# Performance work log

Hardware: AMD Instinct MI355X
Metric: run time of the kernel (lower is better)

The kernel has to match this reference:

```python
import jax, jax.numpy as jnp
import numpy as np

N_NODES = 40000
N_EDGES = 640000
HIDDEN = 128
N_LAYERS = 4
N_CLASSES = 40
SCALING = HIDDEN ** -0.5  # num_heads = 1 -> head_dim = HIDDEN


def setup_inputs() -> dict:
    key = jax.random.key(0)
    ks = jax.random.split(key, 8)
    w_scale = HIDDEN ** -0.5
    h = jax.random.normal(ks[0], (N_NODES, HIDDEN), dtype=jnp.float32)
    src = jax.random.randint(ks[1], (N_EDGES,), 0, N_NODES, dtype=jnp.int32)
    dst = jnp.sort(jax.random.randint(ks[2], (N_EDGES,), 0, N_NODES, dtype=jnp.int32))
    Wq = jax.random.normal(ks[3], (N_LAYERS, HIDDEN, HIDDEN), dtype=jnp.float32) * w_scale
    Wk = jax.random.normal(ks[4], (N_LAYERS, HIDDEN, HIDDEN), dtype=jnp.float32) * w_scale
    Wv = jax.random.normal(ks[5], (N_LAYERS, HIDDEN, HIDDEN), dtype=jnp.float32) * w_scale
    bq = jnp.zeros((N_LAYERS, HIDDEN), dtype=jnp.float32)
    bk = jnp.zeros((N_LAYERS, HIDDEN), dtype=jnp.float32)
    bv = jnp.zeros((N_LAYERS, HIDDEN), dtype=jnp.float32)
    Wout = jax.random.normal(ks[6], (HIDDEN, N_CLASSES), dtype=jnp.float32) * w_scale
    bout = jnp.zeros((N_CLASSES,), dtype=jnp.float32)
    return {"h": h, "src": src, "dst": dst, "Wq": Wq, "bq": bq, "Wk": Wk,
            "bk": bk, "Wv": Wv, "bv": bv, "Wout": Wout, "bout": bout}


def _edge_softmax_spmm(q, k, v, src, dst):
    """Sparse MHA over graph edges (num_heads=1).
    score_e = <q[dst_e], k[src_e]>, softmax over incoming edges per dst,
    out[i] = sum_{e: dst_e = i} attn_e * v[src_e].
    """
    # SDDMM: [E]
    score = jnp.einsum('ed,ed->e', q[dst], k[src])
    # edge softmax over destination segments (stable)
    m = jax.ops.segment_max(score, dst, num_segments=N_NODES)  # [N]
    e = jnp.exp(score - m[dst])                                # [E]
    s = jax.ops.segment_sum(e, dst, num_segments=N_NODES)      # [N]
    attn = e / jnp.maximum(s[dst], 1e-20)                      # [E]
    # SpMM: [N, d]
    return jax.ops.segment_sum(attn[:, None] * v[src], dst, num_segments=N_NODES)


def reference(h, src, dst, Wq, bq, Wk, bk, Wv, bv, Wout, bout):
    for l in range(N_LAYERS):
        q = (h @ Wq[l] + bq[l]) * SCALING
        k = h @ Wk[l] + bk[l]
        v = h @ Wv[l] + bv[l]
        h = _edge_softmax_spmm(q, k, v, src, dst)
    logits = h @ Wout + bout
    return jax.nn.log_softmax(logits, axis=-1)
```

## Files before the change

kernel.cpp:

```cpp
#include <hip/hip_runtime.h>
#include <math.h>

#define N_NODES 40000
#define N_EDGES 640000
#define HIDDEN 128
#define N_LAYERS 4
#define N_CLASSES 40
#define SCALING 0.08838834764831845f

typedef __attribute__((ext_vector_type(8))) short short8;
typedef __attribute__((ext_vector_type(4))) float floatx4;

static __device__ __forceinline__ float b2f(unsigned short u) {
  return __uint_as_float(((unsigned)u) << 16);
}
static __device__ __forceinline__ unsigned short f2b(float f) {
  unsigned u = __float_as_uint(f);
  u += 0x7fff + ((u >> 16) & 1);
  return (unsigned short)(u >> 16);
}

__global__ __launch_bounds__(256) void setup_all(
    const float* __restrict__ h_in, const int* __restrict__ dst,
    unsigned short* __restrict__ g0, int* __restrict__ row_start)
{
  int idx = blockIdx.x * 256 + threadIdx.x;
  if (idx < 640000) {
    const float4* p = (const float4*)h_in + (size_t)idx * 2;
    float4 a = p[0], b = p[1];
    union { unsigned short us[8]; uint4 v; } o;
    o.us[0] = f2b(a.x); o.us[1] = f2b(a.y); o.us[2] = f2b(a.z); o.us[3] = f2b(a.w);
    o.us[4] = f2b(b.x); o.us[5] = f2b(b.y); o.us[6] = f2b(b.z); o.us[7] = f2b(b.w);
    ((uint4*)g0)[idx] = o.v;
    return;
  }
  int c = idx - 640000;
  if (c <= N_NODES) {
    int lo = 0, hi = N_EDGES;
    while (lo < hi) {
      int mid = (lo + hi) >> 1;
      if (dst[mid] < c) lo = mid + 1; else hi = mid;
    }
    row_start[c] = lo;
  }
}

struct MMJob {
  const float* A; const float* B;
  float* Cf; unsigned short* Cb;
  float scale;
  int abt; int ncolsB; int storeT; int padrows;
};
struct MMStage { MMJob jobs[4]; int njobs; int bias; };

__global__ __launch_bounds__(256) void mm_stage(
    MMStage st,
    const float* __restrict__ Wq, const float* __restrict__ Wk,
    const float* __restrict__ Wv, const float* __restrict__ Wout,
    const float* __restrict__ bq, const float* __restrict__ bv,
    const float* __restrict__ bout,
    const float* __restrict__ C2, const float* __restrict__ C3,
    float* __restrict__ zb, float* __restrict__ bout2)
{
  int blk = blockIdx.x;
  if (blk < st.njobs * 64) {
    MMJob J = st.jobs[blk >> 6];
    int bi = blk & 63;
    int ty = threadIdx.x >> 7;
    int c  = threadIdx.x & 127;
    int r  = bi * 2 + ty;
    float acc = 0.f;
    if (J.abt) {
      const float* ar = J.A + (size_t)r * 128;
      const float* br = J.B + (size_t)c * 128;
      #pragma unroll 4
      for (int j = 0; j < 128; ++j) acc += ar[j] * br[j];
    } else if (c < J.ncolsB) {
      const float* ar = J.A + (size_t)r * 128;
      #pragma unroll 4
      for (int j = 0; j < 128; ++j) acc += ar[j] * J.B[(size_t)j * J.ncolsB + c];
    }
    acc *= J.scale;
    if (J.storeT) {
      if (c < J.ncolsB) {
        if (J.Cb) J.Cb[(size_t)c * 128 + r] = f2b(acc);
        else      J.Cf[(size_t)c * 128 + r] = acc;
      } else if (c < J.padrows && J.Cb) {
        J.Cb[(size_t)c * 128 + r] = 0;
      }
    } else if (c < J.ncolsB) {
      if (J.Cb) J.Cb[(size_t)r * J.ncolsB + c] = f2b(acc);
      else      J.Cf[(size_t)r * J.ncolsB + c] = acc;
    }
    return;
  }
  if (!st.bias) return;

  int t = threadIdx.x;
  __shared__ float cb[128], v1[128], v2[128], cbn[128];
  if (t < 128) {
    const float* wk0 = Wk + (size_t)t * 128;
    float s = 0.f;
    for (int o = 0; o < 128; ++o) s += bq[o] * wk0[o];
    zb[t] = s * SCALING;
    cb[t] = bv[t];
  }
  __syncthreads();
  for (int l = 1; l < 4; ++l) {
    const float* Cvl = (l == 1) ? Wv : (l == 2 ? C2 : C3);
    if (t < 128) {
      float s = bq[(size_t)l * 128 + t];
      for (int o = 0; o < 128; ++o) s += cb[o] * Wq[(size_t)l * 16384 + (size_t)o * 128 + t];
      v1[t] = s;
    }
    __syncthreads();
    if (t < 128) {
      float s = 0.f;
      const float* wkr = Wk + (size_t)l * 16384 + (size_t)t * 128;
      for (int o = 0; o < 128; ++o) s += v1[o] * wkr[o];
      v2[t] = s;
    }
    __syncthreads();
    if (t < 128) {
      float s = 0.f;
      const float* cvr = Cvl + (size_t)t * 128;
      for (int d = 0; d < 128; ++d) s += v2[d] * cvr[d];
      zb[(size_t)l * 128 + t] = s * SCALING;
      float s2 = bv[(size_t)l * 128 + t];
      for (int d = 0; d < 128; ++d) s2 += cb[d] * Wv[(size_t)l * 16384 + (size_t)d * 128 + t];
      cbn[t] = s2;
    }
    __syncthreads();
    if (t < 128) cb[t] = cbn[t];
    __syncthreads();
  }
  if (t < N_CLASSES) {
    float s = bout[t];
    for (int d = 0; d < 128; ++d) s += cb[d] * Wout[(size_t)d * N_CLASSES + t];
    bout2[t] = s;
  }
}

__global__ __launch_bounds__(256) void gemm_z(
    const unsigned short* __restrict__ A,
    const unsigned short* __restrict__ Wt,
    const float* __restrict__ bias,
    unsigned short* __restrict__ C)
{
  constexpr int ROWB = 256;
  __shared__ __align__(16) unsigned char cs[32 * ROWB];

  const int tid = threadIdx.x;
  const int wid = tid >> 6, lane = tid & 63;
  const int r = lane & 15, kg = lane >> 4;
  const int colhalf = wid & 1, rowsub = wid >> 1;
  const int colbase = colhalf * 64;
  const int ro = rowsub * 16 + r;
  const int row = blockIdx.x * 32 + ro;

  short8 hf[4];
  #pragma unroll
  for (int kc = 0; kc < 4; ++kc)
    hf[kc] = *(const short8*)(A + (size_t)row * 128 + kc * 32 + kg * 8);

  floatx4 acc[4];
  #pragma unroll
  for (int df = 0; df < 4; ++df) acc[df] = (floatx4){0.f, 0.f, 0.f, 0.f};

  const unsigned short* wp = Wt + (size_t)(colbase + r) * 128 + kg * 8;
  #pragma unroll
  for (int df = 0; df < 4; ++df) {
    #pragma unroll
    for (int kc = 0; kc < 4; ++kc) {
      short8 wf = *(const short8*)(wp + df * 2048 + kc * 32);
      acc[df] = __builtin_amdgcn_mfma_f32_16x16x32_bf16(wf, hf[kc], acc[df], 0, 0, 0);
    }
  }

  #pragma unroll
  for (int df = 0; df < 4; ++df) {
    float4 b4 = *(const float4*)&bias[colbase + df * 16 + kg * 4];
    union { unsigned short us[4]; uint2 u2; } o;
    o.us[0] = f2b(acc[df][0] + b4.x);
    o.us[1] = f2b(acc[df][1] + b4.y);
    o.us[2] = f2b(acc[df][2] + b4.z);
    o.us[3] = f2b(acc[df][3] + b4.w);
    int colb = (colbase + df * 16 + kg * 4) * 2;
    *(uint2*)(cs + ro * ROWB + (colb ^ ((ro & 7) << 4))) = o.u2;
  }
  __syncthreads();

  unsigned char* dstb = (unsigned char*)(C + (size_t)blockIdx.x * 32 * 128);
  #pragma unroll
  for (int i = 0; i < 2; ++i) {
    int byte = (i * 256 + tid) * 16;
    int ro2 = byte / ROWB;
    int colb2 = byte & (ROWB - 1);
    *(uint4*)(dstb + byte) =
        *(const uint4*)(cs + ro2 * ROWB + (colb2 ^ ((ro2 & 7) << 4)));
  }
}

__global__ __launch_bounds__(128) void edge_fused(
    const unsigned short* __restrict__ z, const unsigned short* __restrict__ g,
    const int* __restrict__ src, const int* __restrict__ row_start,
    unsigned short* __restrict__ gout)
{
  const int lane = threadIdx.x & 63;
  const int node = blockIdx.x * 2 + (threadIdx.x >> 6);
  const int sg = lane >> 4, sl = lane & 15;

  short8 qf = *(const short8*)(z + ((size_t)node << 7) + sl * 8);
  float qd[8];
  #pragma unroll
  for (int j = 0; j < 8; ++j) qd[j] = b2f((unsigned short)qf[j]);

  const int r0 = row_start[node], r1 = row_start[node + 1];

  float acc[8] = {0.f, 0.f, 0.f, 0.f, 0.f, 0.f, 0.f, 0.f};
  float ws = 0.f;

#define LOADG(VLD, HF, C)                                               \
  {                                                                     \
    int e_ = (C) + sg;                                                  \
    VLD = e_ < r1;                                                      \
    int s_ = VLD ? src[e_] : 0;                                         \
    HF = *(const short8*)(g + ((size_t)s_ << 7) + sl * 8);              \
  }

#define COMPG(VLD, HF)                                                  \
  {                                                                     \
    float hd_[8];                                                       \
    _Pragma("unroll")                                                   \
    for (int j = 0; j < 8; ++j) hd_[j] = b2f((unsigned short)HF[j]);    \
    float d0_ = 0.f, d1_ = 0.f;                                         \
    _Pragma("unroll")                                                   \
    for (int j = 0; j < 4; ++j) d0_ += qd[j] * hd_[j];                  \
    _Pragma("unroll")                                                   \
    for (int j = 4; j < 8; ++j) d1_ += qd[j] * hd_[j];                  \
    float d_ = d0_ + d1_;                                               \
    d_ += __shfl_xor(d_, 1, 64);                                        \
    d_ += __shfl_xor(d_, 2, 64);                                        \
    d_ += __shfl_xor(d_, 4, 64);                                        \
    d_ += __shfl_xor(d_, 8, 64);                                        \
    float w_ = VLD ? __expf(d_) : 0.f;                                  \
    ws += w_;                                                           \
    _Pragma("unroll")                                                   \
    for (int j = 0; j < 8; ++j) acc[j] += w_ * hd_[j];                  \
  }

  bool vA, vB;
  short8 hA, hB;
  LOADG(vA, hA, r0);
  LOADG(vB, hB, r0 + 4);

  for (int c = r0; c < r1; c += 8) {
    bool vC, vD;
    short8 hC, hD;
    LOADG(vC, hC, c + 8);
    LOADG(vD, hD, c + 12);
    COMPG(vA, hA);
    COMPG(vB, hB);
    vA = vC; hA = hC;
    vB = vD; hB = hD;
  }

#undef LOADG
#undef COMPG

  #pragma unroll
  for (int off = 16; off <= 32; off <<= 1) {
    ws += __shfl_xor(ws, off, 64);
    #pragma unroll
    for (int j = 0; j < 8; ++j) acc[j] += __shfl_xor(acc[j], off, 64);
  }

  if (sg == 0) {
    float inv = (ws > 1e-20f) ? 1.0f / ws : 0.0f;
    union { unsigned short us[8]; uint4 u4; } o;
    #pragma unroll
    for (int j = 0; j < 8; ++j) o.us[j] = f2b(acc[j] * inv);
    *(uint4*)(gout + (size_t)node * 128 + sl * 8) = o.u4;
  }
}

__global__ __launch_bounds__(256) void out_head_mfma(
    const unsigned short* __restrict__ h, const unsigned short* __restrict__ wout_t,
    const float* __restrict__ bout, float* __restrict__ out)
{
  __shared__ __align__(16) float os[64 * N_CLASSES];

  const int wid = threadIdx.x >> 6, lane = threadIdx.x & 63;
  const int r = lane & 15, kg = lane >> 4;
  const int row_base = blockIdx.x * 64 + wid * 16;
  const int ar = row_base + r;

  floatx4 acc[3];
  #pragma unroll
  for (int n = 0; n < 3; ++n) acc[n] = (floatx4){0.f, 0.f, 0.f, 0.f};

  const unsigned short* ap = h + (size_t)ar * 128 + kg * 8;
  const unsigned short* bp = wout_t + (size_t)r * 128 + kg * 8;

  #pragma unroll
  for (int kc = 0; kc < 128; kc += 32) {
    short8 a0 = *(const short8*)(ap + kc);
    #pragma unroll
    for (int n = 0; n < 3; ++n) {
      short8 b = *(const short8*)(bp + n * 2048 + kc);
      acc[n] = __builtin_amdgcn_mfma_f32_16x16x32_bf16(a0, b, acc[n], 0, 0, 0);
    }
  }

  float bn0 = bout[r];
  float bn1 = bout[16 + r];
  float bn2 = (r < 8) ? bout[32 + r] : 0.f;

  #pragma unroll
  for (int g = 0; g < 4; ++g) {
    int rl = wid * 16 + kg * 4 + g;
    float l0 = acc[0][g] + bn0;
    float l1 = acc[1][g] + bn1;
    float l2 = acc[2][g] + bn2;
    float m = fmaxf(l0, l1);
    if (r < 8) m = fmaxf(m, l2);
    #pragma unroll
    for (int off = 8; off >= 1; off >>= 1) m = fmaxf(m, __shfl_xor(m, off, 64));
    float s = __expf(l0 - m) + __expf(l1 - m) + ((r < 8) ? __expf(l2 - m) : 0.f);
    #pragma unroll
    for (int off = 8; off >= 1; off >>= 1) s += __shfl_xor(s, off, 64);
    float lse = m + logf(s);
    os[rl * N_CLASSES + r]      = l0 - lse;
    os[rl * N_CLASSES + 16 + r] = l1 - lse;
    if (r < 8) os[rl * N_CLASSES + 32 + r] = l2 - lse;
  }
  __syncthreads();

  float* dstb = out + (size_t)blockIdx.x * 64 * N_CLASSES;
  #pragma unroll
  for (int i = 0; i < 3; ++i) {
    int idx = i * 256 + threadIdx.x;
    if (idx < 640)
      *(uint4*)(dstb + idx * 4) = *(const uint4*)(os + idx * 4);
  }
}

extern "C" void kernel_launch(void* const* d_in, const int* in_sizes, int n_in,
                              void* d_out, int out_size, void* d_ws, size_t ws_size,
                              hipStream_t stream) {
  const float* h_in = (const float*)d_in[0];
  const int*   src  = (const int*)d_in[1];
  const int*   dst  = (const int*)d_in[2];
  const float* Wq   = (const float*)d_in[3];
  const float* bq   = (const float*)d_in[4];
  const float* Wk   = (const float*)d_in[5];
  const float* bk   = (const float*)d_in[6];
  const float* Wv   = (const float*)d_in[7];
  const float* bv   = (const float*)d_in[8];
  const float* Wout = (const float*)d_in[9];
  const float* bout = (const float*)d_in[10];
  float* out = (float*)d_out;
  (void)bk;

  char* ws = (char*)d_ws;
  size_t off = 0;
  auto alloc = [&](size_t bytes) -> void* {
    void* p = ws + off;
    off += (bytes + 255) & ~(size_t)255;
    return p;
  };
  int*            row_start = (int*)           alloc((size_t)(N_NODES + 1) * sizeof(int));
  unsigned short* g0        = (unsigned short*)alloc((size_t)N_NODES * 128 * 2);
  unsigned short* g1        = (unsigned short*)alloc((size_t)N_NODES * 128 * 2);
  unsigned short* zbuf      = (unsigned short*)alloc((size_t)N_NODES * 128 * 2);
  unsigned short* WZ        = (unsigned short*)alloc((size_t)4 * 16384 * 2);
  unsigned short* WOt       = (unsigned short*)alloc((size_t)48 * 128 * 2);
  float*          C2        = (float*)alloc(16384 * sizeof(float));
  float*          C3        = (float*)alloc(16384 * sizeof(float));
  float*          C4        = (float*)alloc(16384 * sizeof(float));
  float*          Abuf      = (float*)alloc(3 * 16384 * sizeof(float));
  float*          Bbuf      = (float*)alloc(3 * 16384 * sizeof(float));
  float*          zb        = (float*)alloc(4 * 128 * sizeof(float));
  float*          bout2     = (float*)alloc(64 * sizeof(float));

  setup_all<<<(680001 + 255) / 256, 256, 0, stream>>>(h_in, dst, g0, row_start);

  auto J = [](const float* A, const float* B, float* Cf, unsigned short* Cb,
              float scale, int abt, int ncolsB, int storeT, int padrows) {
    MMJob j; j.A = A; j.B = B; j.Cf = Cf; j.Cb = Cb; j.scale = scale;
    j.abt = abt; j.ncolsB = ncolsB; j.storeT = storeT; j.padrows = padrows;
    return j;
  };
  const float* Wq_l[4] = {Wq, Wq + 16384, Wq + 32768, Wq + 49152};
  const float* Wk_l[4] = {Wk, Wk + 16384, Wk + 32768, Wk + 49152};
  const float* Wv_l[4] = {Wv, Wv + 16384, Wv + 32768, Wv + 49152};

  MMStage s0 = {};
  s0.jobs[0] = J(Wk_l[0], Wq_l[0], nullptr, WZ, SCALING, 1, 128, 0, 0);
  s0.jobs[1] = J(Wv_l[0], Wv_l[1], C2, nullptr, 1.f, 0, 128, 0, 0);
  s0.jobs[2] = J(Wv_l[0], Wk_l[1], Abuf, nullptr, 1.f, 0, 128, 0, 0);
  s0.jobs[3] = J(Wv_l[0], Wq_l[1], Bbuf, nullptr, 1.f, 0, 128, 0, 0);
  s0.njobs = 4; s0.bias = 0;

  MMStage s1 = {};
  s1.jobs[0] = J(Abuf, Bbuf, nullptr, WZ + 16384, SCALING, 1, 128, 0, 0);
  s1.jobs[1] = J(C2, Wv_l[2], C3, nullptr, 1.f, 0, 128, 0, 0);
  s1.jobs[2] = J(C2, Wk_l[2], Abuf + 16384, nullptr, 1.f, 0, 128, 0, 0);
  s1.jobs[3] = J(C2, Wq_l[2], Bbuf + 16384, nullptr, 1.f, 0, 128, 0, 0);
  s1.njobs = 4; s1.bias = 0;

  MMStage s2 = {};
  s2.jobs[0] = J(Abuf + 16384, Bbuf + 16384, nullptr, WZ + 32768, SCALING, 1, 128, 0, 0);
  s2.jobs[1] = J(C3, Wv_l[3], C4, nullptr, 1.f, 0, 128, 0, 0);
  s2.jobs[2] = J(C3, Wk_l[3], Abuf + 32768, nullptr, 1.f, 0, 128, 0, 0);
  s2.jobs[3] = J(C3, Wq_l[3], Bbuf + 32768, nullptr, 1.f, 0, 128, 0, 0);
  s2.njobs = 4; s2.bias = 0;

  MMStage s3 = {};
  s3.jobs[0] = J(Abuf + 32768, Bbuf + 32768, nullptr, WZ + 49152, SCALING, 1, 128, 0, 0);
  s3.jobs[1] = J(C4, Wout, nullptr, WOt, 1.f, 0, N_CLASSES, 1, 48);
  s3.njobs = 2; s3.bias = 1;

  mm_stage<<<4 * 64, 256, 0, stream>>>(s0, Wq, Wk, Wv, Wout, bq, bv, bout, C2, C3, zb, bout2);
  mm_stage<<<4 * 64, 256, 0, stream>>>(s1, Wq, Wk, Wv, Wout, bq, bv, bout, C2, C3, zb, bout2);
  mm_stage<<<4 * 64, 256, 0, stream>>>(s2, Wq, Wk, Wv, Wout, bq, bv, bout, C2, C3, zb, bout2);
  mm_stage<<<2 * 64 + 1, 256, 0, stream>>>(s3, Wq, Wk, Wv, Wout, bq, bv, bout, C2, C3, zb, bout2);

  unsigned short* gcur = g0;
  unsigned short* gnext = g1;
  for (int l = 0; l < N_LAYERS; ++l) {
    gemm_z<<<1250, 256, 0, stream>>>(gcur, WZ + (size_t)l * 16384, zb + (size_t)l * 128, zbuf);
    edge_fused<<<N_NODES / 2, 128, 0, stream>>>(zbuf, gcur, src, row_start, gnext);
    unsigned short* tmp = gcur; gcur = gnext; gnext = tmp;
  }
  out_head_mfma<<<625, 256, 0, stream>>>(gcur, WOt, bout2, out);
}
```

Before: 251.5 us.

## Fuse per-layer GEMM into edge aggregation kernel and fold output head into last layer

Merges the gemm_z and edge_fused kernels so each 256-thread block computes the projected query rows for 32 nodes into shared memory and then aggregates neighbours for those nodes. This avoids writing and rereading the z buffer in global memory and saves launches. The final layer keeps its outputs in shared memory and applies the output head with log-softmax in the same kernel. In exchange, each wave now processes 8 nodes serially instead of 1 node per wave across 20000 blocks, which reduces parallelism for latency hiding on the gather and adds load imbalance from varying node degrees.

```diff
diff --git a/kernel.cpp b/kernel.cpp
--- a/kernel.cpp
+++ b/kernel.cpp
@@ -141,89 +141,70 @@
   }
 }
 
-__global__ __launch_bounds__(256) void gemm_z(
-    const unsigned short* __restrict__ A,
+template<bool LAST>
+__global__ __launch_bounds__(256) void layer_fused(
+    const unsigned short* __restrict__ g,
     const unsigned short* __restrict__ Wt,
     const float* __restrict__ bias,
-    unsigned short* __restrict__ C)
+    const int* __restrict__ src, const int* __restrict__ row_start,
+    unsigned short* __restrict__ gout,
+    const unsigned short* __restrict__ WOt,
+    const float* __restrict__ bout2,
+    float* __restrict__ out)
 {
-  constexpr int ROWB = 256;
-  __shared__ __align__(16) unsigned char cs[32 * ROWB];
+  __shared__ __align__(16) unsigned char zs[8192];
+  __shared__ __align__(16) unsigned char gs2[LAST ? 8192 : 16];
+  __shared__ __align__(16) float os[LAST ? 32 * N_CLASSES : 4];
 
   const int tid = threadIdx.x;
   const int wid = tid >> 6, lane = tid & 63;
   const int r = lane & 15, kg = lane >> 4;
-  const int colhalf = wid & 1, rowsub = wid >> 1;
-  const int colbase = colhalf * 64;
-  const int ro = rowsub * 16 + r;
-  const int row = blockIdx.x * 32 + ro;
-
-  short8 hf[4];
-  #pragma unroll
-  for (int kc = 0; kc < 4; ++kc)
-    hf[kc] = *(const short8*)(A + (size_t)row * 128 + kc * 32 + kg * 8);
-
-  floatx4 acc[4];
-  #pragma unroll
-  for (int df = 0; df < 4; ++df) acc[df] = (floatx4){0.f, 0.f, 0.f, 0.f};
-
-  const unsigned short* wp = Wt + (size_t)(colbase + r) * 128 + kg * 8;
-  #pragma unroll
-  for (int df = 0; df < 4; ++df) {
-    #pragma unroll
-    for (int kc = 0; kc < 4; ++kc) {
-      short8 wf = *(const short8*)(wp + df * 2048 + kc * 32);
-      acc[df] = __builtin_amdgcn_mfma_f32_16x16x32_bf16(wf, hf[kc], acc[df], 0, 0, 0);
-    }
-  }
-
-  #pragma unroll
-  for (int df = 0; df < 4; ++df) {
-    float4 b4 = *(const float4*)&bias[colbase + df * 16 + kg * 4];
-    union { unsigned short us[4]; uint2 u2; } o;
-    o.us[0] = f2b(acc[df][0] + b4.x);
-    o.us[1] = f2b(acc[df][1] + b4.y);
-    o.us[2] = f2b(acc[df][2] + b4.z);
-    o.us[3] = f2b(acc[df][3] + b4.w);
-    int colb = (colbase + df * 16 + kg * 4) * 2;
-    *(uint2*)(cs + ro * ROWB + (colb ^ ((ro & 7) << 4))) = o.u2;
+
+  {
+    const int colhalf = wid & 1, rowsub = wid >> 1;
+    const int colbase = colhalf * 64;
+    const int ro = rowsub * 16 + r;
+    const int row = blockIdx.x * 32 + ro;
+
+    short8 hf[4];
+    #pragma unroll
+    for (int kc = 0; kc < 4; ++kc)
+      hf[kc] = *(const short8*)(g + (size_t)row * 128 + kc * 32 + kg * 8);
+
+    floatx4 acc[4];
+    #pragma unroll
+    for (int df = 0; df < 4; ++df) acc[df] = (floatx4){0.f, 0.f, 0.f, 0.f};
+
+    const unsigned short* wp = Wt + (size_t)(colbase + r) * 128 + kg * 8;
+    #pragma unroll
+    for (int df = 0; df < 4; ++df) {
+      #pragma unroll
+      for (int kc = 0; kc < 4; ++kc) {
+        short8 wf = *(const short8*)(wp + df * 2048 + kc * 32);
+        acc[df] = __builtin_amdgcn_mfma_f32_16x16x32_bf16(wf, hf[kc], acc[df], 0, 0, 0);
+      }
+    }
+
+    #pragma unroll
+    for (int df = 0; df < 4; ++df) {
+      float4 b4 = *(const float4*)&bias[colbase + df * 16 + kg * 4];
+      union { unsigned short us[4]; uint2 u2; } o;
+      o.us[0] = f2b(acc[df][0] + b4.x);
+      o.us[1] = f2b(acc[df][1] + b4.y);
+      o.us[2] = f2b(acc[df][2] + b4.z);
+      o.us[3] = f2b(acc[df][3] + b4.w);
+      int colb = (colbase + df * 16 + kg * 4) * 2;
+      *(uint2*)(zs + ro * 256 + (colb ^ ((ro & 7) << 4))) = o.u2;
+    }
   }
   __syncthreads();
 
-  unsigned char* dstb = (unsigned char*)(C + (size_t)blockIdx.x * 32 * 128);
-  #pragma unroll
-  for (int i = 0; i < 2; ++i) {
-    int byte = (i * 256 + tid) * 16;
-    int ro2 = byte / ROWB;
-    int colb2 = byte & (ROWB - 1);
-    *(uint4*)(dstb + byte) =
-        *(const uint4*)(cs + ro2 * ROWB + (colb2 ^ ((ro2 & 7) << 4)));
-  }
-}
-
-__global__ __launch_bounds__(128) void edge_fused(
-    const unsigned short* __restrict__ z, const unsigned short* __restrict__ g,
-    const int* __restrict__ src, const int* __restrict__ row_start,
-    unsigned short* __restrict__ gout)
-{
-  const int lane = threadIdx.x & 63;
-  const int node = blockIdx.x * 2 + (threadIdx.x >> 6);
   const int sg = lane >> 4, sl = lane & 15;
 
-  short8 qf = *(const short8*)(z + ((size_t)node << 7) + sl * 8);
-  float qd[8];
-  #pragma unroll
-  for (int j = 0; j < 8; ++j) qd[j] = b2f((unsigned short)qf[j]);
-
-  const int r0 = row_start[node], r1 = row_start[node + 1];
-
-  float acc[8] = {0.f, 0.f, 0.f, 0.f, 0.f, 0.f, 0.f, 0.f};
-  float ws = 0.f;
-
-#define LOADG(VLD, HF, C)                                               \
+#define LOADG(VLD, HF, C, R1)                                           \
   {                                                                     \
     int e_ = (C) + sg;                                                  \
-    VLD = e_ < r1;                                                      \
+    VLD = e_ < R1;                                                      \
     int s_ = VLD ? src[e_] : 0;                                         \
     HF = *(const short8*)(g + ((size_t)s_ << 7) + sl * 8);              \
   }
@@ -249,98 +230,109 @@
     for (int j = 0; j < 8; ++j) acc[j] += w_ * hd_[j];                  \
   }
 
-  bool vA, vB;
-  short8 hA, hB;
-  LOADG(vA, hA, r0);
-  LOADG(vB, hB, r0 + 4);
-
-  for (int c = r0; c < r1; c += 8) {
-    bool vC, vD;
-    short8 hC, hD;
-    LOADG(vC, hC, c + 8);
-    LOADG(vD, hD, c + 12);
-    COMPG(vA, hA);
-    COMPG(vB, hB);
-    vA = vC; hA = hC;
-    vB = vD; hB = hD;
+  for (int ni = 0; ni < 8; ++ni) {
+    const int nl = wid * 8 + ni;
+    const int node = blockIdx.x * 32 + nl;
+
+    short8 qf = *(const short8*)(zs + nl * 256 + ((sl * 16) ^ ((nl & 7) << 4)));
+    float qd[8];
+    #pragma unroll
+    for (int j = 0; j < 8; ++j) qd[j] = b2f((unsigned short)qf[j]);
+
+    const int r0 = row_start[node], r1 = row_start[node + 1];
+
+    float acc[8] = {0.f, 0.f, 0.f, 0.f, 0.f, 0.f, 0.f, 0.f};
+    float ws = 0.f;
+
+    bool vA, vB;
+    short8 hA, hB;
+    LOADG(vA, hA, r0, r1);
+    LOADG(vB, hB, r0 + 4, r1);
+
+    for (int c = r0; c < r1; c += 8) {
+      bool vC, vD;
+      short8 hC, hD;
+      LOADG(vC, hC, c + 8, r1);
+      LOADG(vD, hD, c + 12, r1);
+      COMPG(vA, hA);
+      COMPG(vB, hB);
+      vA = vC; hA = hC;
+      vB = vD; hB = hD;
+    }
+
+    #pragma unroll
+    for (int off = 16; off <= 32; off <<= 1) {
+      ws += __shfl_xor(ws, off, 64);
+      #pragma unroll
+      for (int j = 0; j < 8; ++j) acc[j] += __shfl_xor(acc[j], off, 64);
+    }
+
+    if (sg == 0) {
+      float inv = (ws > 1e-20f) ? 1.0f / ws : 0.0f;
+      union { unsigned short us[8]; uint4 u4; } o;
+      #pragma unroll
+      for (int j = 0; j < 8; ++j) o.us[j] = f2b(acc[j] * inv);
+      if (LAST)
+        *(uint4*)(gs2 + nl * 256 + ((sl * 16) ^ ((nl & 7) << 4))) = o.u4;
+      else
+        *(uint4*)(gout + (size_t)node * 128 + sl * 8) = o.u4;
+    }
   }
 
 #undef LOADG
 #undef COMPG
 
+  if (!LAST) return;
+
+  __syncthreads();
+  if (wid < 2) {
+    const int rowl = wid * 16 + r;
+    floatx4 acc[3];
+    #pragma unroll
+    for (int n = 0; n < 3; ++n) acc[n] = (floatx4){0.f, 0.f, 0.f, 0.f};
+
+    const unsigned short* bp = WOt + (size_t)r * 128 + kg * 8;
+    #pragma unroll
+    for (int kc = 0; kc < 4; ++kc) {
+      short8 a0 = *(const short8*)(gs2 + rowl * 256 +
+                                   ((kc * 64 + kg * 16) ^ ((rowl & 7) << 4)));
+      #pragma unroll
+      for (int n = 0; n < 3; ++n) {
+        short8 b = *(const short8*)(bp + n * 2048 + kc * 32);
+        acc[n] = __builtin_amdgcn_mfma_f32_16x16x32_bf16(a0, b, acc[n], 0, 0, 0);
+      }
+    }
+
+    float bn0 = bout2[r];
+    float bn1 = bout2[16 + r];
+    float bn2 = (r < 8) ? bout2[32 + r] : 0.f;
+
+    #pragma unroll
+    for (int gi = 0; gi < 4; ++gi) {
+      int rl = wid * 16 + kg * 4 + gi;
+      float l0 = acc[0][gi] + bn0;
+      float l1 = acc[1][gi] + bn1;
+      float l2 = acc[2][gi] + bn2;
+      float m = fmaxf(l0, l1);
+      if (r < 8) m = fmaxf(m, l2);
+      #pragma unroll
+      for (int off = 8; off >= 1; off >>= 1) m = fmaxf(m, __shfl_xor(m, off, 64));
+      float s = __expf(l0 - m) + __expf(l1 - m) + ((r < 8) ? __expf(l2 - m) : 0.f);
+      #pragma unroll
+      for (int off = 8; off >= 1; off >>= 1) s += __shfl_xor(s, off, 64);
+      float lse = m + logf(s);
+      os[rl * N_CLASSES + r]      = l0 - lse;
+      os[rl * N_CLASSES + 16 + r] = l1 - lse;
+      if (r < 8) os[rl * N_CLASSES + 32 + r] = l2 - lse;
+    }
+  }
+  __syncthreads();
+
+  float* dstb = out + (size_t)blockIdx.x * 32 * N_CLASSES;
   #pragma unroll
-  for (int off = 16; off <= 32; off <<= 1) {
-    ws += __shfl_xor(ws, off, 64);
-    #pragma unroll
-    for (int j = 0; j < 8; ++j) acc[j] += __shfl_xor(acc[j], off, 64);
-  }
-
-  if (sg == 0) {
-    float inv = (ws > 1e-20f) ? 1.0f / ws : 0.0f;
-    union { unsigned short us[8]; uint4 u4; } o;
-    #pragma unroll
-    for (int j = 0; j < 8; ++j) o.us[j] = f2b(acc[j] * inv);
-    *(uint4*)(gout + (size_t)node * 128 + sl * 8) = o.u4;
-  }
-}
-
-__global__ __launch_bounds__(256) void out_head_mfma(
-    const unsigned short* __restrict__ h, const unsigned short* __restrict__ wout_t,
-    const float* __restrict__ bout, float* __restrict__ out)
-{
-  __shared__ __align__(16) float os[64 * N_CLASSES];
-
-  const int wid = threadIdx.x >> 6, lane = threadIdx.x & 63;
-  const int r = lane & 15, kg = lane >> 4;
-  const int row_base = blockIdx.x * 64 + wid * 16;
-  const int ar = row_base + r;
-
-  floatx4 acc[3];
-  #pragma unroll
-  for (int n = 0; n < 3; ++n) acc[n] = (floatx4){0.f, 0.f, 0.f, 0.f};
-
-  const unsigned short* ap = h + (size_t)ar * 128 + kg * 8;
-  const unsigned short* bp = wout_t + (size_t)r * 128 + kg * 8;
-
-  #pragma unroll
-  for (int kc = 0; kc < 128; kc += 32) {
-    short8 a0 = *(const short8*)(ap + kc);
-    #pragma unroll
-    for (int n = 0; n < 3; ++n) {
-      short8 b = *(const short8*)(bp + n * 2048 + kc);
-      acc[n] = __builtin_amdgcn_mfma_f32_16x16x32_bf16(a0, b, acc[n], 0, 0, 0);
-    }
-  }
-
-  float bn0 = bout[r];
-  float bn1 = bout[16 + r];
-  float bn2 = (r < 8) ? bout[32 + r] : 0.f;
-
-  #pragma unroll
-  for (int g = 0; g < 4; ++g) {
-    int rl = wid * 16 + kg * 4 + g;
-    float l0 = acc[0][g] + bn0;
-    float l1 = acc[1][g] + bn1;
-    float l2 = acc[2][g] + bn2;
-    float m = fmaxf(l0, l1);
-    if (r < 8) m = fmaxf(m, l2);
-    #pragma unroll
-    for (int off = 8; off >= 1; off >>= 1) m = fmaxf(m, __shfl_xor(m, off, 64));
-    float s = __expf(l0 - m) + __expf(l1 - m) + ((r < 8) ? __expf(l2 - m) : 0.f);
-    #pragma unroll
-    for (int off = 8; off >= 1; off >>= 1) s += __shfl_xor(s, off, 64);
-    float lse = m + logf(s);
-    os[rl * N_CLASSES + r]      = l0 - lse;
-    os[rl * N_CLASSES + 16 + r] = l1 - lse;
-    if (r < 8) os[rl * N_CLASSES + 32 + r] = l2 - lse;
-  }
-  __syncthreads();
-
-  float* dstb = out + (size_t)blockIdx.x * 64 * N_CLASSES;
-  #pragma unroll
-  for (int i = 0; i < 3; ++i) {
-    int idx = i * 256 + threadIdx.x;
-    if (idx < 640)
+  for (int i = 0; i < 2; ++i) {
+    int idx = i * 256 + tid;
+    if (idx < 320)
       *(uint4*)(dstb + idx * 4) = *(const uint4*)(os + idx * 4);
   }
 }
@@ -372,7 +364,6 @@
   int*            row_start = (int*)           alloc((size_t)(N_NODES + 1) * sizeof(int));
   unsigned short* g0        = (unsigned short*)alloc((size_t)N_NODES * 128 * 2);
   unsigned short* g1        = (unsigned short*)alloc((size_t)N_NODES * 128 * 2);
-  unsigned short* zbuf      = (unsigned short*)alloc((size_t)N_NODES * 128 * 2);
   unsigned short* WZ        = (unsigned short*)alloc((size_t)4 * 16384 * 2);
   unsigned short* WOt       = (unsigned short*)alloc((size_t)48 * 128 * 2);
   float*          C2        = (float*)alloc(16384 * sizeof(float));
@@ -426,12 +417,12 @@
   mm_stage<<<4 * 64, 256, 0, stream>>>(s2, Wq, Wk, Wv, Wout, bq, bv, bout, C2, C3, zb, bout2);
   mm_stage<<<2 * 64 + 1, 256, 0, stream>>>(s3, Wq, Wk, Wv, Wout, bq, bv, bout, C2, C3, zb, bout2);
 
-  unsigned short* gcur = g0;
-  unsigned short* gnext = g1;
-  for (int l = 0; l < N_LAYERS; ++l) {
-    gemm_z<<<1250, 256, 0, stream>>>(gcur, WZ + (size_t)l * 16384, zb + (size_t)l * 128, zbuf);
-    edge_fused<<<N_NODES / 2, 128, 0, stream>>>(zbuf, gcur, src, row_start, gnext);
-    unsigned short* tmp = gcur; gcur = gnext; gnext = tmp;
-  }
-  out_head_mfma<<<625, 256, 0, stream>>>(gcur, WOt, bout2, out);
-}
+  layer_fused<false><<<1250, 256, 0, stream>>>(
+      g0, WZ, zb, src, row_start, g1, nullptr, nullptr, nullptr);
+  layer_fused<false><<<1250, 256, 0, stream>>>(
+      g1, WZ + 16384, zb + 128, src, row_start, g0, nullptr, nullptr, nullptr);
+  layer_fused<false><<<1250, 256, 0, stream>>>(
+      g0, WZ + 32768, zb + 256, src, row_start, g1, nullptr, nullptr, nullptr);
+  layer_fused<true><<<1250, 256, 0, stream>>>(
+      g1, WZ + 49152, zb + 384, src, row_start, nullptr, WOt, bout2, out);
+}
```

New measurement: 254.9 us. About the same (+1.4%).

## Fuse weight folding stages, layer-0 gemm, and output head into fewer launches

Applied to the files above, without the earlier changes.

Restructures the weight-product chain into a shallower dependency tree: Wv2·Wv3 and the layer-3 partial products are computed in parallel in the first stage, and the stages are merged with the setup kernel and the layer-0 z GEMM. This cuts kernel launches from 14 to 10. The final SpMM is fused with the output projection and log-softmax, so the last hidden state is never written to memory and the separate head kernel disappears. In exchange, the head is computed with scalar FMAs and shuffles instead of MFMA, and the fused kernels carry heterogeneous block roles.

```diff
diff --git a/kernel.cpp b/kernel.cpp
--- a/kernel.cpp
+++ b/kernel.cpp
@@ -20,124 +20,203 @@
   return (unsigned short)(u >> 16);
 }
 
-__global__ __launch_bounds__(256) void setup_all(
-    const float* __restrict__ h_in, const int* __restrict__ dst,
-    unsigned short* __restrict__ g0, int* __restrict__ row_start)
-{
-  int idx = blockIdx.x * 256 + threadIdx.x;
-  if (idx < 640000) {
-    const float4* p = (const float4*)h_in + (size_t)idx * 2;
-    float4 a = p[0], b = p[1];
-    union { unsigned short us[8]; uint4 v; } o;
-    o.us[0] = f2b(a.x); o.us[1] = f2b(a.y); o.us[2] = f2b(a.z); o.us[3] = f2b(a.w);
-    o.us[4] = f2b(b.x); o.us[5] = f2b(b.y); o.us[6] = f2b(b.z); o.us[7] = f2b(b.w);
-    ((uint4*)g0)[idx] = o.v;
-    return;
-  }
-  int c = idx - 640000;
-  if (c <= N_NODES) {
-    int lo = 0, hi = N_EDGES;
-    while (lo < hi) {
-      int mid = (lo + hi) >> 1;
-      if (dst[mid] < c) lo = mid + 1; else hi = mid;
-    }
-    row_start[c] = lo;
-  }
-}
-
 struct MMJob {
   const float* A; const float* B;
   float* Cf; unsigned short* Cb;
   float scale;
   int abt; int ncolsB; int storeT; int padrows;
 };
-struct MMStage { MMJob jobs[4]; int njobs; int bias; };
-
-__global__ __launch_bounds__(256) void mm_stage(
-    MMStage st,
+struct MM7 { MMJob j[7]; };
+struct MM3 { MMJob j[3]; };
+
+static __device__ __forceinline__ void run_job(const MMJob J, int bi) {
+  int ty = threadIdx.x >> 7;
+  int c  = threadIdx.x & 127;
+  int r  = bi * 2 + ty;
+  float acc = 0.f;
+  if (J.abt) {
+    const float* ar = J.A + (size_t)r * 128;
+    const float* br = J.B + (size_t)c * 128;
+    #pragma unroll 4
+    for (int j = 0; j < 128; ++j) acc += ar[j] * br[j];
+  } else if (c < J.ncolsB) {
+    const float* ar = J.A + (size_t)r * 128;
+    #pragma unroll 4
+    for (int j = 0; j < 128; ++j) acc += ar[j] * J.B[(size_t)j * J.ncolsB + c];
+  }
+  acc *= J.scale;
+  if (J.storeT) {
+    if (c < J.ncolsB) {
+      if (J.Cb) J.Cb[(size_t)c * 128 + r] = f2b(acc);
+      else      J.Cf[(size_t)c * 128 + r] = acc;
+    } else if (c < J.padrows && J.Cb) {
+      J.Cb[(size_t)c * 128 + r] = 0;
+    }
+  } else if (c < J.ncolsB) {
+    if (J.Cb) J.Cb[(size_t)r * J.ncolsB + c] = f2b(acc);
+    else      J.Cf[(size_t)r * J.ncolsB + c] = acc;
+  }
+}
+
+__global__ __launch_bounds__(256) void setup_fold1(
+    const float* __restrict__ h_in, const int* __restrict__ dst,
+    const float* __restrict__ bq, const float* __restrict__ Wk,
+    unsigned short* __restrict__ g0, int* __restrict__ row_start,
+    float* __restrict__ zb, MM7 st)
+{
+  int blk = blockIdx.x;
+  if (blk < 2657) {
+    int idx = blk * 256 + threadIdx.x;
+    if (idx < 640000) {
+      const float4* p = (const float4*)h_in + (size_t)idx * 2;
+      float4 a = p[0], b = p[1];
+      union { unsigned short us[8]; uint4 v; } o;
+      o.us[0] = f2b(a.x); o.us[1] = f2b(a.y); o.us[2] = f2b(a.z); o.us[3] = f2b(a.w);
+      o.us[4] = f2b(b.x); o.us[5] = f2b(b.y); o.us[6] = f2b(b.z); o.us[7] = f2b(b.w);
+      ((uint4*)g0)[idx] = o.v;
+      return;
+    }
+    int c = idx - 640000;
+    if (c <= N_NODES) {
+      int lo = 0, hi = N_EDGES;
+      while (lo < hi) {
+        int mid = (lo + hi) >> 1;
+        if (dst[mid] < c) lo = mid + 1; else hi = mid;
+      }
+      row_start[c] = lo;
+    }
+    return;
+  }
+  if (blk < 3105) {
+    int b2 = blk - 2657;
+    run_job(st.j[b2 >> 6], b2 & 63);
+    return;
+  }
+  int t = threadIdx.x;
+  if (t < 128) {
+    const float* wkr = Wk + (size_t)t * 128;
+    float s = 0.f;
+    #pragma unroll 4
+    for (int o = 0; o < 128; ++o) s += bq[o] * wkr[o];
+    zb[t] = s * SCALING;
+  }
+}
+
+__global__ __launch_bounds__(256) void fold2(MM7 st) {
+  run_job(st.j[blockIdx.x >> 6], blockIdx.x & 63);
+}
+
+__global__ __launch_bounds__(256) void fold3_z0(
+    MM3 st,
     const float* __restrict__ Wq, const float* __restrict__ Wk,
     const float* __restrict__ Wv, const float* __restrict__ Wout,
     const float* __restrict__ bq, const float* __restrict__ bv,
     const float* __restrict__ bout,
-    const float* __restrict__ C2, const float* __restrict__ C3,
-    float* __restrict__ zb, float* __restrict__ bout2)
+    const float* __restrict__ D01, const float* __restrict__ C3f,
+    float* __restrict__ zb, float* __restrict__ bout2,
+    const unsigned short* __restrict__ g, const unsigned short* __restrict__ WZ0,
+    unsigned short* __restrict__ zout)
 {
   int blk = blockIdx.x;
-  if (blk < st.njobs * 64) {
-    MMJob J = st.jobs[blk >> 6];
-    int bi = blk & 63;
-    int ty = threadIdx.x >> 7;
-    int c  = threadIdx.x & 127;
-    int r  = bi * 2 + ty;
-    float acc = 0.f;
-    if (J.abt) {
-      const float* ar = J.A + (size_t)r * 128;
-      const float* br = J.B + (size_t)c * 128;
-      #pragma unroll 4
-      for (int j = 0; j < 128; ++j) acc += ar[j] * br[j];
-    } else if (c < J.ncolsB) {
-      const float* ar = J.A + (size_t)r * 128;
-      #pragma unroll 4
-      for (int j = 0; j < 128; ++j) acc += ar[j] * J.B[(size_t)j * J.ncolsB + c];
-    }
-    acc *= J.scale;
-    if (J.storeT) {
-      if (c < J.ncolsB) {
-        if (J.Cb) J.Cb[(size_t)c * 128 + r] = f2b(acc);
-        else      J.Cf[(size_t)c * 128 + r] = acc;
-      } else if (c < J.padrows && J.Cb) {
-        J.Cb[(size_t)c * 128 + r] = 0;
+  if (blk < 192) {
+    run_job(st.j[blk >> 6], blk & 63);
+    return;
+  }
+  if (blk == 192) {
+    int t = threadIdx.x;
+    __shared__ float cb[128], v1[128], v2[128], cbn[128];
+    if (t < 128) cb[t] = bv[t];
+    __syncthreads();
+    for (int l = 1; l < 4; ++l) {
+      const float* Cvl = (l == 1) ? Wv : (l == 2 ? D01 : C3f);
+      if (t < 128) {
+        float s = bq[(size_t)l * 128 + t];
+        for (int o = 0; o < 128; ++o) s += cb[o] * Wq[(size_t)l * 16384 + (size_t)o * 128 + t];
+        v1[t] = s;
       }
-    } else if (c < J.ncolsB) {
-      if (J.Cb) J.Cb[(size_t)r * J.ncolsB + c] = f2b(acc);
-      else      J.Cf[(size_t)r * J.ncolsB + c] = acc;
+      __syncthreads();
+      if (t < 128) {
+        float s = 0.f;
+        const float* wkr = Wk + (size_t)l * 16384 + (size_t)t * 128;
+        for (int o = 0; o < 128; ++o) s += v1[o] * wkr[o];
+        v2[t] = s;
+      }
+      __syncthreads();
+      if (t < 128) {
+        float s = 0.f;
+        const float* cvr = Cvl + (size_t)t * 128;
+        for (int d = 0; d < 128; ++d) s += v2[d] * cvr[d];
+        zb[(size_t)l * 128 + t] = s * SCALING;
+        float s2 = bv[(size_t)l * 128 + t];
+        for (int d = 0; d < 128; ++d) s2 += cb[d] * Wv[(size_t)l * 16384 + (size_t)d * 128 + t];
+        cbn[t] = s2;
+      }
+      __syncthreads();
+      if (t < 128) cb[t] = cbn[t];
+      __syncthreads();
+    }
+    if (t < N_CLASSES) {
+      float s = bout[t];
+      for (int d = 0; d < 128; ++d) s += cb[d] * Wout[(size_t)d * N_CLASSES + t];
+      bout2[t] = s;
     }
     return;
   }
-  if (!st.bias) return;
-
-  int t = threadIdx.x;
-  __shared__ float cb[128], v1[128], v2[128], cbn[128];
-  if (t < 128) {
-    const float* wk0 = Wk + (size_t)t * 128;
-    float s = 0.f;
-    for (int o = 0; o < 128; ++o) s += bq[o] * wk0[o];
-    zb[t] = s * SCALING;
-    cb[t] = bv[t];
-  }
-  __syncthreads();
-  for (int l = 1; l < 4; ++l) {
-    const float* Cvl = (l == 1) ? Wv : (l == 2 ? C2 : C3);
-    if (t < 128) {
-      float s = bq[(size_t)l * 128 + t];
-      for (int o = 0; o < 128; ++o) s += cb[o] * Wq[(size_t)l * 16384 + (size_t)o * 128 + t];
-      v1[t] = s;
+
+  {
+    const int tile = blk - 193;
+    constexpr int ROWB = 256;
+    __shared__ __align__(16) unsigned char cs[32 * ROWB];
+
+    const int tid = threadIdx.x;
+    const int wid = tid >> 6, lane = tid & 63;
+    const int r = lane & 15, kg = lane >> 4;
+    const int colhalf = wid & 1, rowsub = wid >> 1;
+    const int colbase = colhalf * 64;
+    const int ro = rowsub * 16 + r;
+    const int row = tile * 32 + ro;
+
+    short8 hf[4];
+    #pragma unroll
+    for (int kc = 0; kc < 4; ++kc)
+      hf[kc] = *(const short8*)(g + (size_t)row * 128 + kc * 32 + kg * 8);
+
+    floatx4 acc[4];
+    #pragma unroll
+    for (int df = 0; df < 4; ++df) acc[df] = (floatx4){0.f, 0.f, 0.f, 0.f};
+
+    const unsigned short* wp = WZ0 + (size_t)(colbase + r) * 128 + kg * 8;
+    #pragma unroll
+    for (int df = 0; df < 4; ++df) {
+      #pragma unroll
+      for (int kc = 0; kc < 4; ++kc) {
+        short8 wf = *(const short8*)(wp + df * 2048 + kc * 32);
+        acc[df] = __builtin_amdgcn_mfma_f32_16x16x32_bf16(wf, hf[kc], acc[df], 0, 0, 0);
+      }
+    }
+
+    #pragma unroll
+    for (int df = 0; df < 4; ++df) {
+      float4 b4 = *(const float4*)&zb[colbase + df * 16 + kg * 4];
+      union { unsigned short us[4]; uint2 u2; } o;
+      o.us[0] = f2b(acc[df][0] + b4.x);
+      o.us[1] = f2b(acc[df][1] + b4.y);
+      o.us[2] = f2b(acc[df][2] + b4.z);
+      o.us[3] = f2b(acc[df][3] + b4.w);
+      int colb = (colbase + df * 16 + kg * 4) * 2;
+      *(uint2*)(cs + ro * ROWB + (colb ^ ((ro & 7) << 4))) = o.u2;
     }
     __syncthreads();
-    if (t < 128) {
-      float s = 0.f;
-      const float* wkr = Wk + (size_t)l * 16384 + (size_t)t * 128;
-      for (int o = 0; o < 128; ++o) s += v1[o] * wkr[o];
-      v2[t] = s;
-    }
-    __syncthreads();
-    if (t < 128) {
-      float s = 0.f;
-      const float* cvr = Cvl + (size_t)t * 128;
-      for (int d = 0; d < 128; ++d) s += v2[d] * cvr[d];
-      zb[(size_t)l * 128 + t] = s * SCALING;
-      float s2 = bv[(size_t)l * 128 + t];
-      for (int d = 0; d < 128; ++d) s2 += cb[d] * Wv[(size_t)l * 16384 + (size_t)d * 128 + t];
-      cbn[t] = s2;
-    }
-    __syncthreads();
-    if (t < 128) cb[t] = cbn[t];
-    __syncthreads();
-  }
-  if (t < N_CLASSES) {
-    float s = bout[t];
-    for (int d = 0; d < 128; ++d) s += cb[d] * Wout[(size_t)d * N_CLASSES + t];
-    bout2[t] = s;
+
+    unsigned char* dstb = (unsigned char*)(zout + (size_t)tile * 32 * 128);
+    #pragma unroll
+    for (int i = 0; i < 2; ++i) {
+      int byte = (i * 256 + tid) * 16;
+      int ro2 = byte / ROWB;
+      int colb2 = byte & (ROWB - 1);
+      *(uint4*)(dstb + byte) =
+          *(const uint4*)(cs + ro2 * ROWB + (colb2 ^ ((ro2 & 7) << 4)));
+    }
   }
 }
 
@@ -201,26 +280,7 @@
   }
 }
 
-__global__ __launch_bounds__(128) void edge_fused(
-    const unsigned short* __restrict__ z, const unsigned short* __restrict__ g,
-    const int* __restrict__ src, const int* __restrict__ row_start,
-    unsigned short* __restrict__ gout)
-{
-  const int lane = threadIdx.x & 63;
-  const int node = blockIdx.x * 2 + (threadIdx.x >> 6);
-  const int sg = lane >> 4, sl = lane & 15;
-
-  short8 qf = *(const short8*)(z + ((size_t)node << 7) + sl * 8);
-  float qd[8];
-  #pragma unroll
-  for (int j = 0; j < 8; ++j) qd[j] = b2f((unsigned short)qf[j]);
-
-  const int r0 = row_start[node], r1 = row_start[node + 1];
-
-  float acc[8] = {0.f, 0.f, 0.f, 0.f, 0.f, 0.f, 0.f, 0.f};
-  float ws = 0.f;
-
-#define LOADG(VLD, HF, C)                                               \
+#define EDGE_LOADG(VLD, HF, C)                                          \
   {                                                                     \
     int e_ = (C) + sg;                                                  \
     VLD = e_ < r1;                                                      \
@@ -228,7 +288,7 @@
     HF = *(const short8*)(g + ((size_t)s_ << 7) + sl * 8);              \
   }
 
-#define COMPG(VLD, HF)                                                  \
+#define EDGE_COMPG(VLD, HF)                                             \
   {                                                                     \
     float hd_[8];                                                       \
     _Pragma("unroll")                                                   \
@@ -249,31 +309,47 @@
     for (int j = 0; j < 8; ++j) acc[j] += w_ * hd_[j];                  \
   }
 
-  bool vA, vB;
-  short8 hA, hB;
-  LOADG(vA, hA, r0);
-  LOADG(vB, hB, r0 + 4);
-
-  for (int c = r0; c < r1; c += 8) {
-    bool vC, vD;
-    short8 hC, hD;
-    LOADG(vC, hC, c + 8);
-    LOADG(vD, hD, c + 12);
-    COMPG(vA, hA);
-    COMPG(vB, hB);
-    vA = vC; hA = hC;
-    vB = vD; hB = hD;
-  }
-
-#undef LOADG
-#undef COMPG
-
-  #pragma unroll
-  for (int off = 16; off <= 32; off <<= 1) {
-    ws += __shfl_xor(ws, off, 64);
-    #pragma unroll
-    for (int j = 0; j < 8; ++j) acc[j] += __shfl_xor(acc[j], off, 64);
-  }
+#define EDGE_BODY                                                       \
+  float acc[8] = {0.f, 0.f, 0.f, 0.f, 0.f, 0.f, 0.f, 0.f};              \
+  float ws = 0.f;                                                       \
+  bool vA, vB;                                                          \
+  short8 hA, hB;                                                        \
+  EDGE_LOADG(vA, hA, r0);                                               \
+  EDGE_LOADG(vB, hB, r0 + 4);                                           \
+  for (int c = r0; c < r1; c += 8) {                                    \
+    bool vC, vD;                                                        \
+    short8 hC, hD;                                                      \
+    EDGE_LOADG(vC, hC, c + 8);                                          \
+    EDGE_LOADG(vD, hD, c + 12);                                         \
+    EDGE_COMPG(vA, hA);                                                 \
+    EDGE_COMPG(vB, hB);                                                 \
+    vA = vC; hA = hC;                                                   \
+    vB = vD; hB = hD;                                                   \
+  }                                                                     \
+  _Pragma("unroll")                                                     \
+  for (int off = 16; off <= 32; off <<= 1) {                            \
+    ws += __shfl_xor(ws, off, 64);                                      \
+    _Pragma("unroll")                                                   \
+    for (int j = 0; j < 8; ++j) acc[j] += __shfl_xor(acc[j], off, 64);  \
+  }
+
+__global__ __launch_bounds__(128) void edge_fused(
+    const unsigned short* __restrict__ z, const unsigned short* __restrict__ g,
+    const int* __restrict__ src, const int* __restrict__ row_start,
+    unsigned short* __restrict__ gout)
+{
+  const int lane = threadIdx.x & 63;
+  const int node = blockIdx.x * 2 + (threadIdx.x >> 6);
+  const int sg = lane >> 4, sl = lane & 15;
+
+  short8 qf = *(const short8*)(z + ((size_t)node << 7) + sl * 8);
+  float qd[8];
+  #pragma unroll
+  for (int j = 0; j < 8; ++j) qd[j] = b2f((unsigned short)qf[j]);
+
+  const int r0 = row_start[node], r1 = row_start[node + 1];
+
+  EDGE_BODY
 
   if (sg == 0) {
     float inv = (ws > 1e-20f) ? 1.0f / ws : 0.0f;
@@ -284,66 +360,64 @@
   }
 }
 
-__global__ __launch_bounds__(256) void out_head_mfma(
-    const unsigned short* __restrict__ h, const unsigned short* __restrict__ wout_t,
-    const float* __restrict__ bout, float* __restrict__ out)
+__global__ __launch_bounds__(128) void edge_head(
+    const unsigned short* __restrict__ z, const unsigned short* __restrict__ g,
+    const int* __restrict__ src, const int* __restrict__ row_start,
+    const unsigned short* __restrict__ WOt, const float* __restrict__ bout2,
+    float* __restrict__ out)
 {
-  __shared__ __align__(16) float os[64 * N_CLASSES];
-
-  const int wid = threadIdx.x >> 6, lane = threadIdx.x & 63;
-  const int r = lane & 15, kg = lane >> 4;
-  const int row_base = blockIdx.x * 64 + wid * 16;
-  const int ar = row_base + r;
-
-  floatx4 acc[3];
-  #pragma unroll
-  for (int n = 0; n < 3; ++n) acc[n] = (floatx4){0.f, 0.f, 0.f, 0.f};
-
-  const unsigned short* ap = h + (size_t)ar * 128 + kg * 8;
-  const unsigned short* bp = wout_t + (size_t)r * 128 + kg * 8;
-
-  #pragma unroll
-  for (int kc = 0; kc < 128; kc += 32) {
-    short8 a0 = *(const short8*)(ap + kc);
-    #pragma unroll
-    for (int n = 0; n < 3; ++n) {
-      short8 b = *(const short8*)(bp + n * 2048 + kc);
-      acc[n] = __builtin_amdgcn_mfma_f32_16x16x32_bf16(a0, b, acc[n], 0, 0, 0);
-    }
-  }
-
-  float bn0 = bout[r];
-  float bn1 = bout[16 + r];
-  float bn2 = (r < 8) ? bout[32 + r] : 0.f;
-
-  #pragma unroll
-  for (int g = 0; g < 4; ++g) {
-    int rl = wid * 16 + kg * 4 + g;
-    float l0 = acc[0][g] + bn0;
-    float l1 = acc[1][g] + bn1;
-    float l2 = acc[2][g] + bn2;
-    float m = fmaxf(l0, l1);
-    if (r < 8) m = fmaxf(m, l2);
-    #pragma unroll
-    for (int off = 8; off >= 1; off >>= 1) m = fmaxf(m, __shfl_xor(m, off, 64));
-    float s = __expf(l0 - m) + __expf(l1 - m) + ((r < 8) ? __expf(l2 - m) : 0.f);
-    #pragma unroll
-    for (int off = 8; off >= 1; off >>= 1) s += __shfl_xor(s, off, 64);
-    float lse = m + logf(s);
-    os[rl * N_CLASSES + r]      = l0 - lse;
-    os[rl * N_CLASSES + 16 + r] = l1 - lse;
-    if (r < 8) os[rl * N_CLASSES + 32 + r] = l2 - lse;
-  }
-  __syncthreads();
-
-  float* dstb = out + (size_t)blockIdx.x * 64 * N_CLASSES;
-  #pragma unroll
-  for (int i = 0; i < 3; ++i) {
-    int idx = i * 256 + threadIdx.x;
-    if (idx < 640)
-      *(uint4*)(dstb + idx * 4) = *(const uint4*)(os + idx * 4);
-  }
-}
+  const int lane = threadIdx.x & 63;
+  const int node = blockIdx.x * 2 + (threadIdx.x >> 6);
+  const int sg = lane >> 4, sl = lane & 15;
+
+  short8 qf = *(const short8*)(z + ((size_t)node << 7) + sl * 8);
+  float qd[8];
+  #pragma unroll
+  for (int j = 0; j < 8; ++j) qd[j] = b2f((unsigned short)qf[j]);
+
+  const int r0 = row_start[node], r1 = row_start[node + 1];
+
+  EDGE_BODY
+
+  float inv = (ws > 1e-20f) ? 1.0f / ws : 0.0f;
+
+  float cls[10];
+  #pragma unroll
+  for (int it = 0; it < 10; ++it) {
+    int c = sg * 10 + it;
+    short8 w = *(const short8*)(WOt + (size_t)c * 128 + sl * 8);
+    float p = 0.f;
+    #pragma unroll
+    for (int j = 0; j < 8; ++j) p += acc[j] * b2f((unsigned short)w[j]);
+    p += __shfl_xor(p, 1, 64);
+    p += __shfl_xor(p, 2, 64);
+    p += __shfl_xor(p, 4, 64);
+    p += __shfl_xor(p, 8, 64);
+    cls[it] = p * inv + bout2[c];
+  }
+  float m = cls[0];
+  #pragma unroll
+  for (int it = 1; it < 10; ++it) m = fmaxf(m, cls[it]);
+  m = fmaxf(m, __shfl_xor(m, 16, 64));
+  m = fmaxf(m, __shfl_xor(m, 32, 64));
+  float s = 0.f;
+  #pragma unroll
+  for (int it = 0; it < 10; ++it) s += __expf(cls[it] - m);
+  s += __shfl_xor(s, 16, 64);
+  s += __shfl_xor(s, 32, 64);
+  float lse = m + logf(s);
+
+  if (sl < 10) {
+    float v = cls[0];
+    #pragma unroll
+    for (int it = 1; it < 10; ++it) if (sl == it) v = cls[it];
+    out[(size_t)node * N_CLASSES + sg * 10 + sl] = v - lse;
+  }
+}
+
+#undef EDGE_BODY
+#undef EDGE_COMPG
+#undef EDGE_LOADG
 
 extern "C" void kernel_launch(void* const* d_in, const int* in_sizes, int n_in,
                               void* d_out, int out_size, void* d_ws, size_t ws_size,
@@ -375,15 +449,20 @@
   unsigned short* zbuf      = (unsigned short*)alloc((size_t)N_NODES * 128 * 2);
   unsigned short* WZ        = (unsigned short*)alloc((size_t)4 * 16384 * 2);
   unsigned short* WOt       = (unsigned short*)alloc((size_t)48 * 128 * 2);
-  float*          C2        = (float*)alloc(16384 * sizeof(float));
-  float*          C3        = (float*)alloc(16384 * sizeof(float));
-  float*          C4        = (float*)alloc(16384 * sizeof(float));
-  float*          Abuf      = (float*)alloc(3 * 16384 * sizeof(float));
-  float*          Bbuf      = (float*)alloc(3 * 16384 * sizeof(float));
-  float*          zb        = (float*)alloc(4 * 128 * sizeof(float));
-  float*          bout2     = (float*)alloc(64 * sizeof(float));
-
-  setup_all<<<(680001 + 255) / 256, 256, 0, stream>>>(h_in, dst, g0, row_start);
+  float*          D01  = (float*)alloc(16384 * 4);
+  float*          D23  = (float*)alloc(16384 * 4);
+  float*          A1f  = (float*)alloc(16384 * 4);
+  float*          B1f  = (float*)alloc(16384 * 4);
+  float*          E3   = (float*)alloc(16384 * 4);
+  float*          F3   = (float*)alloc(16384 * 4);
+  float*          A2f  = (float*)alloc(16384 * 4);
+  float*          B2f  = (float*)alloc(16384 * 4);
+  float*          A3f  = (float*)alloc(16384 * 4);
+  float*          B3f  = (float*)alloc(16384 * 4);
+  float*          C4f  = (float*)alloc(16384 * 4);
+  float*          C3f  = (float*)alloc(16384 * 4);
+  float*          zb   = (float*)alloc(4 * 128 * 4);
+  float*          bout2 = (float*)alloc(64 * 4);
 
   auto J = [](const float* A, const float* B, float* Cf, unsigned short* Cb,
               float scale, int abt, int ncolsB, int storeT, int padrows) {
@@ -395,43 +474,39 @@
   const float* Wk_l[4] = {Wk, Wk + 16384, Wk + 32768, Wk + 49152};
   const float* Wv_l[4] = {Wv, Wv + 16384, Wv + 32768, Wv + 49152};
 
-  MMStage s0 = {};
-  s0.jobs[0] = J(Wk_l[0], Wq_l[0], nullptr, WZ, SCALING, 1, 128, 0, 0);
-  s0.jobs[1] = J(Wv_l[0], Wv_l[1], C2, nullptr, 1.f, 0, 128, 0, 0);
-  s0.jobs[2] = J(Wv_l[0], Wk_l[1], Abuf, nullptr, 1.f, 0, 128, 0, 0);
-  s0.jobs[3] = J(Wv_l[0], Wq_l[1], Bbuf, nullptr, 1.f, 0, 128, 0, 0);
-  s0.njobs = 4; s0.bias = 0;
-
-  MMStage s1 = {};
-  s1.jobs[0] = J(Abuf, Bbuf, nullptr, WZ + 16384, SCALING, 1, 128, 0, 0);
-  s1.jobs[1] = J(C2, Wv_l[2], C3, nullptr, 1.f, 0, 128, 0, 0);
-  s1.jobs[2] = J(C2, Wk_l[2], Abuf + 16384, nullptr, 1.f, 0, 128, 0, 0);
-  s1.jobs[3] = J(C2, Wq_l[2], Bbuf + 16384, nullptr, 1.f, 0, 128, 0, 0);
-  s1.njobs = 4; s1.bias = 0;
-
-  MMStage s2 = {};
-  s2.jobs[0] = J(Abuf + 16384, Bbuf + 16384, nullptr, WZ + 32768, SCALING, 1, 128, 0, 0);
-  s2.jobs[1] = J(C3, Wv_l[3], C4, nullptr, 1.f, 0, 128, 0, 0);
-  s2.jobs[2] = J(C3, Wk_l[3], Abuf + 32768, nullptr, 1.f, 0, 128, 0, 0);
-  s2.jobs[3] = J(C3, Wq_l[3], Bbuf + 32768, nullptr, 1.f, 0, 128, 0, 0);
-  s2.njobs = 4; s2.bias = 0;
-
-  MMStage s3 = {};
-  s3.jobs[0] = J(Abuf + 32768, Bbuf + 32768, nullptr, WZ + 49152, SCALING, 1, 128, 0, 0);
-  s3.jobs[1] = J(C4, Wout, nullptr, WOt, 1.f, 0, N_CLASSES, 1, 48);
-  s3.njobs = 2; s3.bias = 1;
-
-  mm_stage<<<4 * 64, 256, 0, stream>>>(s0, Wq, Wk, Wv, Wout, bq, bv, bout, C2, C3, zb, bout2);
-  mm_stage<<<4 * 64, 256, 0, stream>>>(s1, Wq, Wk, Wv, Wout, bq, bv, bout, C2, C3, zb, bout2);
-  mm_stage<<<4 * 64, 256, 0, stream>>>(s2, Wq, Wk, Wv, Wout, bq, bv, bout, C2, C3, zb, bout2);
-  mm_stage<<<2 * 64 + 1, 256, 0, stream>>>(s3, Wq, Wk, Wv, Wout, bq, bv, bout, C2, C3, zb, bout2);
-
-  unsigned short* gcur = g0;
-  unsigned short* gnext = g1;
-  for (int l = 0; l < N_LAYERS; ++l) {
-    gemm_z<<<1250, 256, 0, stream>>>(gcur, WZ + (size_t)l * 16384, zb + (size_t)l * 128, zbuf);
-    edge_fused<<<N_NODES / 2, 128, 0, stream>>>(zbuf, gcur, src, row_start, gnext);
-    unsigned short* tmp = gcur; gcur = gnext; gnext = tmp;
-  }
-  out_head_mfma<<<625, 256, 0, stream>>>(gcur, WOt, bout2, out);
-}
+  MM7 s1;
+  s1.j[0] = J(Wk_l[0], Wq_l[0], nullptr, WZ, SCALING, 1, 128, 0, 0);
+  s1.j[1] = J(Wv_l[0], Wv_l[1], D01, nullptr, 1.f, 0, 128, 0, 0);
+  s1.j[2] = J(Wv_l[2], Wv_l[3], D23, nullptr, 1.f, 0, 128, 0, 0);
+  s1.j[3] = J(Wv_l[0], Wk_l[1], A1f, nullptr, 1.f, 0, 128, 0, 0);
+  s1.j[4] = J(Wv_l[0], Wq_l[1], B1f, nullptr, 1.f, 0, 128, 0, 0);
+  s1.j[5] = J(Wv_l[2], Wk_l[3], E3,  nullptr, 1.f, 0, 128, 0, 0);
+  s1.j[6] = J(Wv_l[2], Wq_l[3], F3,  nullptr, 1.f, 0, 128, 0, 0);
+
+  MM7 s2;
+  s2.j[0] = J(A1f, B1f, nullptr, WZ + 16384, SCALING, 1, 128, 0, 0);
+  s2.j[1] = J(D01, Wk_l[2], A2f, nullptr, 1.f, 0, 128, 0, 0);
+  s2.j[2] = J(D01, Wq_l[2], B2f, nullptr, 1.f, 0, 128, 0, 0);
+  s2.j[3] = J(D01, E3, A3f, nullptr, 1.f, 0, 128, 0, 0);
+  s2.j[4] = J(D01, F3, B3f, nullptr, 1.f, 0, 128, 0, 0);
+  s2.j[5] = J(D01, D23, C4f, nullptr, 1.f, 0, 128, 0, 0);
+  s2.j[6] = J(D01, Wv_l[2], C3f, nullptr, 1.f, 0, 128, 0, 0);
+
+  MM3 s3;
+  s3.j[0] = J(A2f, B2f, nullptr, WZ + 32768, SCALING, 1, 128, 0, 0);
+  s3.j[1] = J(A3f, B3f, nullptr, WZ + 49152, SCALING, 1, 128, 0, 0);
+  s3.j[2] = J(C4f, Wout, nullptr, WOt, 1.f, 0, N_CLASSES, 1, 48);
+
+  setup_fold1<<<3106, 256, 0, stream>>>(h_in, dst, bq, Wk, g0, row_start, zb, s1);
+  fold2<<<448, 256, 0, stream>>>(s2);
+  fold3_z0<<<1443, 256, 0, stream>>>(s3, Wq, Wk, Wv, Wout, bq, bv, bout,
+                                     D01, C3f, zb, bout2, g0, WZ, zbuf);
+
+  edge_fused<<<N_NODES / 2, 128, 0, stream>>>(zbuf, g0, src, row_start, g1);
+  gemm_z<<<1250, 256, 0, stream>>>(g1, WZ + 16384, zb + 128, zbuf);
+  edge_fused<<<N_NODES / 2, 128, 0, stream>>>(zbuf, g1, src, row_start, g0);
+  gemm_z<<<1250, 256, 0, stream>>>(g0, WZ + 32768, zb + 256, zbuf);
+  edge_fused<<<N_NODES / 2, 128, 0, stream>>>(zbuf, g0, src, row_start, g1);
+  gemm_z<<<1250, 256, 0, stream>>>(g1, WZ + 49152, zb + 384, zbuf);
+  edge_head<<<N_NODES / 2, 128, 0, stream>>>(zbuf, g1, src, row_start, WOt, bout2, out);
+}
```

New measurement: 241.5 us. 4.0% less time.
